# Kernel optimization log

Hardware: AMD Instinct MI355X
Metric: run time of the kernel (lower is better)

## Reference

```python
import jax, jax.numpy as jnp
import numpy as np

N = 65536      # total nodes (cells) in batch
E = 262144     # edges per edge type
T = 3          # edge types: row, col, diag
D = 128        # hidden_dim
HG = 4         # gat_heads
DHG = D // HG  # 32, GAT head dim
HH = 4         # hgt_heads
DHH = D // HH  # 32, HGT head dim
B = 32         # boards per batch
SLOPE = 0.2
EPS = 1e-6


def setup_inputs():
    ks = jax.random.split(jax.random.key(0), 32)
    def nrm(i, shape, s=0.05):
        return (jax.random.normal(ks[i], shape) * s).astype(jnp.float32)
    inp = {
        'x_cell': nrm(0, (N, D), 1.0),
        'z_h': nrm(1, (B, D), 1.0),
        'x_cell_embedded': nrm(2, (N, D), 1.0),
        'edge_index': jax.random.randint(ks[3], (T, 2, E), 0, N, dtype=jnp.int32),
        'batch_size': B,
        # GAT conv 1 (one GATConv per edge type, summed)
        'gat1_W': nrm(4, (T, D, D), 0.09),
        'gat1_asrc': nrm(5, (T, HG, DHG), 0.12),
        'gat1_adst': nrm(6, (T, HG, DHG), 0.12),
        'gat1_b': jnp.zeros((T, D), jnp.float32),
        # GAT conv 2
        'gat2_W': nrm(7, (T, D, D), 0.09),
        'gat2_asrc': nrm(8, (T, HG, DHG), 0.12),
        'gat2_adst': nrm(9, (T, HG, DHG), 0.12),
        'gat2_b': jnp.zeros((T, D), jnp.float32),
        # RMSNorms
        'norm1_s': jnp.ones((D,), jnp.float32),
        'norm2_s': jnp.ones((D,), jnp.float32),
        'norm3_s': jnp.ones((D,), jnp.float32),
        # HGT (single node type 'cell', T edge types)
        'hgt_Wk': nrm(10, (D, D), 0.09), 'hgt_bk': jnp.zeros((D,), jnp.float32),
        'hgt_Wq': nrm(11, (D, D), 0.09), 'hgt_bq': jnp.zeros((D,), jnp.float32),
        'hgt_Wv': nrm(12, (D, D), 0.09), 'hgt_bv': jnp.zeros((D,), jnp.float32),
        'hgt_arel': nrm(13, (T, HH, DHH, DHH), 0.15),
        'hgt_mrel': nrm(14, (T, HH, DHH, DHH), 0.15),
        'hgt_prel': jnp.ones((T, HH), jnp.float32),
        'hgt_Wo': nrm(15, (D, D), 0.09), 'hgt_bo': jnp.zeros((D,), jnp.float32),
        'hgt_skip': jnp.ones((), jnp.float32),
        # input injection
        'inj_W': nrm(16, (D, D), 0.09), 'inj_b': jnp.zeros((D,), jnp.float32),
        # FiLM
        'film_W1': nrm(17, (D, 2 * D), 0.09), 'film_b1': jnp.zeros((2 * D,), jnp.float32),
        'film_W2': nrm(18, (2 * D, 2 * D), 0.001), 'film_b2': jnp.zeros((2 * D,), jnp.float32),
    }
    return inp


def _rmsnorm(x, scale):
    return scale * x * jax.lax.rsqrt(jnp.mean(x * x, axis=-1, keepdims=True) + EPS)


def _res(x_old, x_new, scale):
    return jax.nn.leaky_relu(x_old + _rmsnorm(x_new, scale), SLOPE)


def _gat_sum(x, W, asrc, adst, b, src, dst):
    """HeteroConv(sum) over T GATConvs (concat heads, add_self_loops)."""
    loop = jnp.arange(N, dtype=src.dtype)
    def one(Wt, a_s, a_d, bt, s, t):
        s = jnp.concatenate([s, loop])   # self loops
        t = jnp.concatenate([t, loop])
        h = (x @ Wt).reshape(N, HG, DHG)             # [N,H,Dh]
        alpha_src = (h * a_s).sum(-1)                # [N,H]
        alpha_dst = (h * a_d).sum(-1)
        e = jax.nn.leaky_relu(alpha_src[s] + alpha_dst[t], SLOPE)  # [E+N,H]
        m = jax.ops.segment_max(e, t, num_segments=N)
        ex = jnp.exp(e - m[t])
        denom = jax.ops.segment_sum(ex, t, num_segments=N)
        alpha = ex / (denom[t] + 1e-16)
        out = jax.ops.segment_sum(alpha[:, :, None] * h[s], t, num_segments=N)
        return out.reshape(N, D) + bt
    return jax.vmap(one)(W, asrc, adst, b, src, dst).sum(0)


def _hgt(x, Wk, bk, Wq, bq, Wv, bv, a_rel, m_rel, p_rel, Wo, bo, skip, src, dst):
    k = (x @ Wk + bk).reshape(N, HH, DHH)
    q = (x @ Wq + bq).reshape(N, HH, DHH)
    v = (x @ Wv + bv).reshape(N, HH, DHH)
    # per-edge-type relation transforms at node level, then gather per edge
    k_t = jnp.einsum('nhd,thdf->tnhf', k, a_rel)    # [T,N,H,Dk]
    v_t = jnp.einsum('nhd,thdf->tnhf', v, m_rel)
    k_e = jax.vmap(lambda a, i: a[i])(k_t, src)     # [T,E,H,Dk]
    v_e = jax.vmap(lambda a, i: a[i])(v_t, src)
    score = (q[dst] * k_e).sum(-1) * p_rel[:, None, :] / np.sqrt(DHH)  # [T,E,H]
    score = score.reshape(T * E, HH)
    dst_f = dst.reshape(-1)
    m = jax.ops.segment_max(score, dst_f, num_segments=N)
    ex = jnp.exp(score - m[dst_f])
    denom = jax.ops.segment_sum(ex, dst_f, num_segments=N)
    alpha = ex / (denom[dst_f] + 1e-16)
    agg = jax.ops.segment_sum(alpha[:, :, None] * v_e.reshape(T * E, HH, DHH),
                              dst_f, num_segments=N)          # [N,H,Dk]
    out = jax.nn.gelu(agg.reshape(N, D), approximate=False) @ Wo + bo
    sig = jax.nn.sigmoid(skip)
    return sig * out + (1.0 - sig) * x


def _film(nodes, z_h, W1, b1, W2, b2, bsz):
    gb = jax.nn.gelu(z_h @ W1 + b1, approximate=False) @ W2 + b2  # [B,2D]
    gamma, beta = jnp.split(gb, 2, axis=-1)
    gamma = 0.1 * jnp.tanh(gamma)
    beta = 0.1 * jnp.tanh(beta)
    c = N // bsz
    out = (1.0 + gamma)[:, None, :] * nodes.reshape(bsz, c, D) + beta[:, None, :]
    return out.reshape(N, D)


def reference(x_cell, z_h, x_cell_embedded,
              gat1_W, gat1_asrc, gat1_adst, gat1_b,
              gat2_W, gat2_asrc, gat2_adst, gat2_b,
              norm1_s, norm2_s, norm3_s,
              hgt_Wk, hgt_bk, hgt_Wq, hgt_bq, hgt_Wv, hgt_bv,
              hgt_arel, hgt_mrel, hgt_prel, hgt_Wo, hgt_bo, hgt_skip,
              inj_W, inj_b, film_W1, film_b1, film_W2, film_b2,
              edge_index, batch_size):
    src = edge_index[:, 0]
    dst = edge_index[:, 1]
    x1 = _res(x_cell, _gat_sum(x_cell, gat1_W, gat1_asrc, gat1_adst, gat1_b, src, dst), norm1_s)
    x2 = _res(x1, _gat_sum(x1, gat2_W, gat2_asrc, gat2_adst, gat2_b, src, dst), norm2_s)
    x3 = _res(x2, _hgt(x2, hgt_Wk, hgt_bk, hgt_Wq, hgt_bq, hgt_Wv, hgt_bv,
                       hgt_arel, hgt_mrel, hgt_prel, hgt_Wo, hgt_bo, hgt_skip,
                       src, dst), norm3_s)
    x3 = x3 + x_cell_embedded @ inj_W + inj_b
    return _film(x3, z_h, film_W1, film_b1, film_W2, film_b2, batch_size)
```

## Files before the change

### kernel.cpp

```cpp
#include <hip/hip_runtime.h>

#define NN 65536
#define EE 262144
#define ND ((size_t)NN * 128)
#define TBW 132

typedef unsigned short u16;
typedef short bf8_t __attribute__((ext_vector_type(8)));
typedef float f32x4 __attribute__((ext_vector_type(4)));

__device__ __forceinline__ float lrelu(float x){ return x > 0.f ? x : 0.2f*x; }
__device__ __forceinline__ float gelu_exact(float x){ return 0.5f*x*(1.f+erff(x*0.70710678118654752f)); }
__device__ __forceinline__ u16 f2bf(float f){
    union { float f; unsigned u; } v; v.f = f;
    unsigned u = v.u;
    return (u16)((u + 0x7FFFu + ((u >> 16) & 1u)) >> 16);
}
__device__ __forceinline__ float bf2f(u16 b){
    union { unsigned u; float f; } v; v.u = ((unsigned)b) << 16; return v.f;
}
__device__ __forceinline__ float2 bf2x(unsigned p){
    union { unsigned u; float f; } a, b;
    a.u = (p & 0xFFFFu) << 16; b.u = p & 0xFFFF0000u;
    return make_float2(a.f, b.f);
}
__device__ __forceinline__ unsigned cvt2(float a, float b){
    unsigned r; asm("v_cvt_pk_bf16_f32 %0, %1, %2" : "=v"(r) : "v"(a), "v"(b)); return r;
}

__device__ __forceinline__ void load_af32(const float* __restrict__ X, int row, int lk, bf8_t* af){
    #pragma unroll
    for (int kk = 0; kk < 4; ++kk){
        const float* p = X + (size_t)row*128 + kk*32 + lk*8;
        float4 a = *(const float4*)p;
        float4 b = *(const float4*)(p+4);
        union { bf8_t v; unsigned u[4]; } r;
        r.u[0] = cvt2(a.x, a.y); r.u[1] = cvt2(a.z, a.w);
        r.u[2] = cvt2(b.x, b.y); r.u[3] = cvt2(b.z, b.w);
        af[kk] = r.v;
    }
}
__device__ __forceinline__ void load_af16(const u16* __restrict__ X, int row, int lk, bf8_t* af){
    #pragma unroll
    for (int kk = 0; kk < 4; ++kk)
        af[kk] = *(const bf8_t*)(X + (size_t)row*128 + kk*32 + lk*8);
}
__device__ __forceinline__ void mfma_w1_acc(const bf8_t* af, const u16* __restrict__ Wp,
                                            int lr, int lk, f32x4* acc){
    #pragma unroll
    for (int kk = 0; kk < 4; ++kk){
        bf8_t B[8];
        #pragma unroll
        for (int nt = 0; nt < 8; ++nt)
            B[nt] = *(const bf8_t*)&Wp[(nt*16+lr)*128 + kk*32 + lk*8];
        #pragma unroll
        for (int nt = 0; nt < 8; ++nt)
            acc[nt] = __builtin_amdgcn_mfma_f32_16x16x32_bf16(af[kk], B[nt], acc[nt], 0, 0, 0);
    }
}
__device__ __forceinline__ void mfma_w1(const bf8_t* af, const u16* __restrict__ Wp,
                                        int lr, int lk, f32x4* acc){
    #pragma unroll
    for (int i = 0; i < 8; ++i) acc[i] = (f32x4){0.f,0.f,0.f,0.f};
    mfma_w1_acc(af, Wp, lr, lk, acc);
}
__device__ __forceinline__ void mfma_w2_acc(const bf8_t* af0, const bf8_t* af1,
                                            const u16* __restrict__ Wp,
                                            int lr, int lk, f32x4* acc0, f32x4* acc1){
    #pragma unroll
    for (int kk = 0; kk < 4; ++kk){
        bf8_t B[8];
        #pragma unroll
        for (int nt = 0; nt < 8; ++nt)
            B[nt] = *(const bf8_t*)&Wp[(nt*16+lr)*128 + kk*32 + lk*8];
        #pragma unroll
        for (int nt = 0; nt < 8; ++nt){
            acc0[nt] = __builtin_amdgcn_mfma_f32_16x16x32_bf16(af0[kk], B[nt], acc0[nt], 0, 0, 0);
            acc1[nt] = __builtin_amdgcn_mfma_f32_16x16x32_bf16(af1[kk], B[nt], acc1[nt], 0, 0, 0);
        }
    }
}
__device__ __forceinline__ void mfma_w2(const bf8_t* af0, const bf8_t* af1,
                                        const u16* __restrict__ Wp,
                                        int lr, int lk, f32x4* acc0, f32x4* acc1){
    #pragma unroll
    for (int i = 0; i < 8; ++i){ acc0[i] = (f32x4){0.f,0.f,0.f,0.f}; acc1[i] = (f32x4){0.f,0.f,0.f,0.f}; }
    mfma_w2_acc(af0, af1, Wp, lr, lk, acc0, acc1);
}
__device__ __forceinline__ void acc_to_tb(u16 (*tbw)[TBW], const f32x4* acc, int lr, int lk, const float* bias){
    asm volatile("s_waitcnt lgkmcnt(0)" ::: "memory");
    #pragma unroll
    for (int nt = 0; nt < 8; ++nt){
        int col = nt*16 + lr;
        float badd = bias ? bias[col] : 0.f;
        #pragma unroll
        for (int i = 0; i < 4; ++i) tbw[lk*4+i][col] = f2bf(acc[nt][i] + badd);
    }
    asm volatile("s_waitcnt lgkmcnt(0)" ::: "memory");
}
__device__ __forceinline__ void acc_to_tb_gelu(u16 (*tbw)[TBW], const f32x4* acc, int lr, int lk){
    asm volatile("s_waitcnt lgkmcnt(0)" ::: "memory");
    #pragma unroll
    for (int nt = 0; nt < 8; ++nt){
        int col = nt*16 + lr;
        #pragma unroll
        for (int i = 0; i < 4; ++i) tbw[lk*4+i][col] = f2bf(gelu_exact(acc[nt][i]));
    }
    asm volatile("s_waitcnt lgkmcnt(0)" ::: "memory");
}
__device__ __forceinline__ void tb_store(const u16 (*tbw)[TBW], u16* __restrict__ O, size_t rowstride, int rowbase, int lr, int lk){
    #pragma unroll
    for (int c = 0; c < 4; ++c){
        bf8_t v = *(const bf8_t*)&tbw[c*4+lk][lr*8];
        *(bf8_t*)(O + (size_t)(rowbase + c*4 + lk)*rowstride + lr*8) = v;
    }
}
__device__ __forceinline__ void tb_frags(const u16 (*tbw)[TBW], int lr, int lk, bf8_t* ha){
    #pragma unroll
    for (int kk = 0; kk < 4; ++kk) ha[kk] = *(const bf8_t*)&tbw[lr][kk*32 + lk*8];
}
__device__ __forceinline__ void tb_rows(const u16 (*tbw)[TBW], int lr, int lk, bf8_t* rw){
    #pragma unroll
    for (int c = 0; c < 4; ++c) rw[c] = *(const bf8_t*)&tbw[c*4+lk][lr*8];
}

__global__ __launch_bounds__(256) void wpack_k(
    const float* __restrict__ g1W, const float* __restrict__ g2W,
    const float* __restrict__ Wk, const float* __restrict__ Wq, const float* __restrict__ Wv,
    const float* __restrict__ Wo, const float* __restrict__ injW,
    const float* __restrict__ arel, const float* __restrict__ mrel,
    const float* __restrict__ g1as, const float* __restrict__ g1ad,
    const float* __restrict__ g2as, const float* __restrict__ g2ad,
    u16* __restrict__ wp, u16* __restrict__ wpa)
{
    int b = blockIdx.x, tid = threadIdx.x;
    if (b < 17) {
        const float* src; int rel = 0;
        if (b < 3) src = g1W + b*16384;
        else if (b < 6) src = g2W + (b-3)*16384;
        else if (b == 6) src = Wk;
        else if (b == 7) src = Wq;
        else if (b == 8) src = Wv;
        else if (b == 9) src = Wo;
        else if (b == 10) src = injW;
        else if (b < 14) { src = arel + (b-11)*4096; rel = 2; }
        else { src = mrel + (b-14)*4096; rel = 1; }
        u16* dst = wp + (size_t)b*16384;
        for (int idx = tid; idx < 16384; idx += 256) {
            int n = idx >> 7, k = idx & 127;
            float v;
            if (rel == 1)      v = ((n>>5)==(k>>5)) ? src[(n>>5)*1024 + (k&31)*32 + (n&31)] : 0.f;
            else if (rel == 2) v = ((n>>5)==(k>>5)) ? src[(n>>5)*1024 + (n&31)*32 + (k&31)] : 0.f;
            else               v = src[k*128 + n];
            dst[idx] = f2bf(v);
        }
    } else {
        for (int idx = tid; idx < 6*2048; idx += 256) {
            int m = idx >> 11;
            int j = idx & 2047;
            int cg = j >> 7, k = j & 127;
            const float* as = (m < 3) ? g1as : g2as;
            const float* ad = (m < 3) ? g1ad : g2ad;
            int t = (m < 3) ? m : m - 3;
            float v = 0.f;
            if (cg < 4)      { if ((k>>5)==cg)   v = as[t*128 + cg*32 + (k&31)]; }
            else if (cg < 8) { int g = cg-4; if ((k>>5)==g) v = ad[t*128 + g*32 + (k&31)]; }
            wpa[idx] = f2bf(v);
        }
    }
}

template<int AF32>
__global__ __launch_bounds__(256, 2) void gat_gemm3_k(const float* __restrict__ Xf, const u16* __restrict__ Xb,
    const u16* __restrict__ wpg, const u16* __restrict__ wpa,
    u16* __restrict__ hb, float* __restrict__ alsb, float* __restrict__ aldb)
{
    __shared__ u16 tb[4][16][TBW];
    const int tid = threadIdx.x, wave = tid>>6, lane = tid&63, lr = lane&15, lk = lane>>4;
    const int rw0 = blockIdx.x*128 + wave*32;
    bf8_t af0[4], af1[4];
    if (AF32){ load_af32(Xf, rw0 + lr, lk, af0); load_af32(Xf, rw0 + 16 + lr, lk, af1); }
    else     { load_af16(Xb, rw0 + lr, lk, af0); load_af16(Xb, rw0 + 16 + lr, lk, af1); }
    f32x4 acc0[8], acc1[8];
    for (int t = 0; t < 3; ++t) {
        mfma_w2(af0, af1, wpg + t*16384, lr, lk, acc0, acc1);
        bf8_t Ba[4];
        #pragma unroll
        for (int kk = 0; kk < 4; ++kk)
            Ba[kk] = *(const bf8_t*)&wpa[t*2048 + lr*128 + kk*32 + lk*8];
        u16* h = hb + (size_t)t*ND;
        float* alst = alsb + (size_t)t*NN*4;
        float* aldt = aldb + (size_t)t*NN*4;
        {
            acc_to_tb(tb[wave], acc0, lr, lk, nullptr);
            tb_store(tb[wave], h, 128, rw0, lr, lk);
            bf8_t ha[4]; tb_frags(tb[wave], lr, lk, ha);
            f32x4 a2 = (f32x4){0.f,0.f,0.f,0.f};
            #pragma unroll
            for (int kk = 0; kk < 4; ++kk)
                a2 = __builtin_amdgcn_mfma_f32_16x16x32_bf16(ha[kk], Ba[kk], a2, 0, 0, 0);
            if (lr < 8){
                float* dp = (lr < 4) ? alst : aldt;
                int g = lr & 3;
                #pragma unroll
                for (int i = 0; i < 4; ++i) dp[(size_t)(rw0 + lk*4 + i)*4 + g] = a2[i];
            }
        }
        {
            acc_to_tb(tb[wave], acc1, lr, lk, nullptr);
            tb_store(tb[wave], h, 128, rw0 + 16, lr, lk);
            bf8_t ha[4]; tb_frags(tb[wave], lr, lk, ha);
            f32x4 a2 = (f32x4){0.f,0.f,0.f,0.f};
            #pragma unroll
            for (int kk = 0; kk < 4; ++kk)
                a2 = __builtin_amdgcn_mfma_f32_16x16x32_bf16(ha[kk], Ba[kk], a2, 0, 0, 0);
            if (lr < 8){
                float* dp = (lr < 4) ? alst : aldt;
                int g = lr & 3;
                #pragma unroll
                for (int i = 0; i < 4; ++i) dp[(size_t)(rw0 + 16 + lk*4 + i)*4 + g] = a2[i];
            }
        }
    }
}

__global__ __launch_bounds__(256, 2) void hgt_proj_k(const u16* __restrict__ X,
    const u16* __restrict__ wpk, const u16* __restrict__ wpq, const u16* __restrict__ wpv,
    const u16* __restrict__ wparel,
    const float* __restrict__ bk, const float* __restrict__ bq, const float* __restrict__ bv,
    u16* __restrict__ kvb, u16* __restrict__ qtb)
{
    __shared__ u16 tb[4][16][TBW];
    const int tid = threadIdx.x, wave = tid>>6, lane = tid&63, lr = lane&15, lk = lane>>4;
    const int rw0 = blockIdx.x*128 + wave*32;
    bf8_t af0[4], af1[4];
    load_af16(X, rw0 + lr, lk, af0);
    load_af16(X, rw0 + 16 + lr, lk, af1);
    f32x4 acc0[8], acc1[8];
    mfma_w2(af0, af1, wpk, lr, lk, acc0, acc1);
    acc_to_tb(tb[wave], acc0, lr, lk, bk); tb_store(tb[wave], kvb, 256, rw0, lr, lk);
    acc_to_tb(tb[wave], acc1, lr, lk, bk); tb_store(tb[wave], kvb, 256, rw0 + 16, lr, lk);
    mfma_w2(af0, af1, wpv, lr, lk, acc0, acc1);
    acc_to_tb(tb[wave], acc0, lr, lk, bv); tb_store(tb[wave], kvb + 128, 256, rw0, lr, lk);
    acc_to_tb(tb[wave], acc1, lr, lk, bv); tb_store(tb[wave], kvb + 128, 256, rw0 + 16, lr, lk);
    bf8_t ha0[4], ha1[4];
    mfma_w2(af0, af1, wpq, lr, lk, acc0, acc1);
    acc_to_tb(tb[wave], acc0, lr, lk, bq); tb_frags(tb[wave], lr, lk, ha0);
    acc_to_tb(tb[wave], acc1, lr, lk, bq); tb_frags(tb[wave], lr, lk, ha1);
    for (int t = 0; t < 3; ++t){
        mfma_w2(ha0, ha1, wparel + t*16384, lr, lk, acc0, acc1);
        u16* o = qtb + (size_t)t*ND;
        acc_to_tb(tb[wave], acc0, lr, lk, nullptr); tb_store(tb[wave], o, 128, rw0, lr, lk);
        acc_to_tb(tb[wave], acc1, lr, lk, nullptr); tb_store(tb[wave], o, 128, rw0 + 16, lr, lk);
    }
}

__global__ __launch_bounds__(256) void hgt_agg_k(const u16* __restrict__ kvb,
    const u16* __restrict__ qtb, const float* __restrict__ prel,
    const int* __restrict__ coff, const int* __restrict__ csrc,
    u16* __restrict__ pb)
{
    int gid = blockIdx.x*256 + threadIdx.x;
    int node = gid >> 6, lane = gid & 63;
    int hh = lane >> 4;
    float a0[3], a1[3];
    float dsum = 0.f;
    #pragma unroll
    for (int t = 0; t < 3; ++t) {
        a0[t] = 0.f; a1[t] = 0.f;
        float ph = prel[t*4 + hh] * 0.17677669529663689f;
        float2 qv = bf2x(*(const unsigned*)&qtb[(size_t)t*ND + (size_t)node*128 + lane*2]);
        const int* cs = csrc + (size_t)t*EE;
        int beg = coff[t*(NN+1) + node], end = coff[t*(NN+1) + node + 1];
        int e = beg;
        for (; e + 4 <= end; e += 4) {
            int sA = cs[e], sB = cs[e+1], sC = cs[e+2], sD = cs[e+3];
            size_t rA = (size_t)sA*256 + lane*2, rB = (size_t)sB*256 + lane*2;
            size_t rC = (size_t)sC*256 + lane*2, rD = (size_t)sD*256 + lane*2;
            unsigned kA = *(const unsigned*)&kvb[rA], kB = *(const unsigned*)&kvb[rB];
            unsigned kC = *(const unsigned*)&kvb[rC], kD = *(const unsigned*)&kvb[rD];
            unsigned vA = *(const unsigned*)&kvb[rA+128], vB = *(const unsigned*)&kvb[rB+128];
            unsigned vC = *(const unsigned*)&kvb[rC+128], vD = *(const unsigned*)&kvb[rD+128];
            float2 k2A = bf2x(kA), k2B = bf2x(kB), k2C = bf2x(kC), k2D = bf2x(kD);
            float scA = qv.x*k2A.x + qv.y*k2A.y;
            float scB = qv.x*k2B.x + qv.y*k2B.y;
            float scC = qv.x*k2C.x + qv.y*k2C.y;
            float scD = qv.x*k2D.x + qv.y*k2D.y;
            #pragma unroll
            for (int o = 1; o < 16; o <<= 1){
                scA += __shfl_xor(scA, o); scB += __shfl_xor(scB, o);
                scC += __shfl_xor(scC, o); scD += __shfl_xor(scD, o);
            }
            float eA = expf(scA*ph), eB = expf(scB*ph), eC = expf(scC*ph), eD = expf(scD*ph);
            float2 v2A = bf2x(vA), v2B = bf2x(vB), v2C = bf2x(vC), v2D = bf2x(vD);
            dsum += eA + eB + eC + eD;
            a0[t] += eA*v2A.x + eB*v2B.x + eC*v2C.x + eD*v2D.x;
            a1[t] += eA*v2A.y + eB*v2B.y + eC*v2C.y + eD*v2D.y;
        }
        for (; e < end; ++e) {
            int s = cs[e];
            size_t ro = (size_t)s*256 + lane*2;
            float2 kv = bf2x(*(const unsigned*)&kvb[ro]);
            float sc = qv.x*kv.x + qv.y*kv.y;
            #pragma unroll
            for (int o = 1; o < 16; o <<= 1) sc += __shfl_xor(sc, o);
            float ex = expf(sc * ph);
            float2 vx = bf2x(*(const unsigned*)&kvb[ro + 128]);
            dsum += ex; a0[t] += ex*vx.x; a1[t] += ex*vx.y;
        }
    }
    float inv = 1.f/(dsum + 1e-16f);
    size_t o = (size_t)node*128 + lane*2;
    #pragma unroll
    for (int t = 0; t < 3; ++t)
        *(unsigned*)&pb[(size_t)t*ND + o] = cvt2(a0[t]*inv, a1[t]*inv);
}

__global__ __launch_bounds__(256, 2) void final_k(const u16* __restrict__ pb,
    const u16* __restrict__ wpmrel, const u16* __restrict__ wpo, const float* __restrict__ bo,
    const u16* __restrict__ x2b, const float* __restrict__ skipp, const float* __restrict__ scale,
    const float* __restrict__ xemb, const u16* __restrict__ wpinj, const float* __restrict__ injb,
    const float* __restrict__ gbuf, const int* __restrict__ bszp,
    float* __restrict__ out)
{
    __shared__ u16 tb[4][2][16][TBW];
    const int tid = threadIdx.x, wave = tid>>6, lane = tid&63, lr = lane&15, lk = lane>>4;
    const int rw0 = blockIdx.x*128 + wave*32;
    const int rw1 = rw0 + 16;
    f32x4 acc0[8], acc1[8];
    #pragma unroll
    for (int i = 0; i < 8; ++i){ acc0[i] = (f32x4){0.f,0.f,0.f,0.f}; acc1[i] = (f32x4){0.f,0.f,0.f,0.f}; }
    for (int t = 0; t < 3; ++t){
        bf8_t a0[4], a1[4];
        load_af16(pb + (size_t)t*ND, rw0 + lr, lk, a0);
        load_af16(pb + (size_t)t*ND, rw1 + lr, lk, a1);
        mfma_w2_acc(a0, a1, wpmrel + t*16384, lr, lk, acc0, acc1);
    }
    acc_to_tb_gelu(tb[wave][0], acc0, lr, lk);
    acc_to_tb_gelu(tb[wave][1], acc1, lr, lk);
    bf8_t ga0[4], ga1[4];
    tb_frags(tb[wave][0], lr, lk, ga0);
    tb_frags(tb[wave][1], lr, lk, ga1);
    mfma_w2(ga0, ga1, wpo, lr, lk, acc0, acc1);
    acc_to_tb(tb[wave][0], acc0, lr, lk, bo);
    acc_to_tb(tb[wave][1], acc1, lr, lk, bo);
    bf8_t hw0[4], hw1[4];
    tb_rows(tb[wave][0], lr, lk, hw0);
    tb_rows(tb[wave][1], lr, lk, hw1);
    bf8_t e0[4], e1[4];
    load_af32(xemb, rw0 + lr, lk, e0);
    load_af32(xemb, rw1 + lr, lk, e1);
    mfma_w2(e0, e1, wpinj, lr, lk, acc0, acc1);
    acc_to_tb(tb[wave][0], acc0, lr, lk, injb);
    acc_to_tb(tb[wave][1], acc1, lr, lk, injb);
    bf8_t in0[4], in1[4];
    tb_rows(tb[wave][0], lr, lk, in0);
    tb_rows(tb[wave][1], lr, lk, in1);
    const float sig = 1.f/(1.f + expf(-skipp[0]));
    const int cpb = NN / *bszp;
    float4 sca = *(const float4*)&scale[lr*8];
    float4 scb = *(const float4*)&scale[lr*8 + 4];
    #pragma unroll
    for (int tile = 0; tile < 2; ++tile){
        const bf8_t* hw = tile ? hw1 : hw0;
        const bf8_t* in = tile ? in1 : in0;
        int rwb = tile ? rw1 : rw0;
        #pragma unroll
        for (int c = 0; c < 4; ++c){
            int row = rwb + c*4 + lk;
            bf8_t x8 = *(const bf8_t*)(x2b + (size_t)row*128 + lr*8);
            float x[8], v[8];
            float ssl = 0.f;
            #pragma unroll
            for (int j = 0; j < 8; ++j){
                x[j] = bf2f((u16)x8[j]);
                float h = bf2f((u16)hw[c][j]);
                v[j] = sig*h + (1.f - sig)*x[j];
                ssl += v[j]*v[j];
            }
            ssl += __shfl_xor(ssl, 1); ssl += __shfl_xor(ssl, 2);
            ssl += __shfl_xor(ssl, 4); ssl += __shfl_xor(ssl, 8);
            float rq = rsqrtf(ssl*(1.f/128.f) + 1e-6f);
            const float* gr = gbuf + (row / cpb)*256;
            float4 g0 = *(const float4*)&gr[lr*8];
            float4 g1 = *(const float4*)&gr[lr*8 + 4];
            float4 b0 = *(const float4*)&gr[128 + lr*8];
            float4 b1 = *(const float4*)&gr[128 + lr*8 + 4];
            float4 oA, oB;
            #pragma unroll
            for (int j = 0; j < 8; ++j){
                float scj = (j < 4) ? ((const float*)&sca)[j] : ((const float*)&scb)[j-4];
                float y = lrelu(x[j] + scj*v[j]*rq);
                float hf = y + bf2f((u16)in[c][j]);
                float gj = (j < 4) ? ((const float*)&g0)[j] : ((const float*)&g1)[j-4];
                float bj = (j < 4) ? ((const float*)&b0)[j] : ((const float*)&b1)[j-4];
                float ov = (1.f + gj)*hf + bj;
                if (j < 4) ((float*)&oA)[j] = ov; else ((float*)&oB)[j-4] = ov;
            }
            *(float4*)(out + (size_t)row*128 + lr*8)     = oA;
            *(float4*)(out + (size_t)row*128 + lr*8 + 4) = oB;
        }
    }
}

__global__ __launch_bounds__(256) void hist_k(const int* __restrict__ ei, int* __restrict__ cnt){
    int gid = blockIdx.x*256 + threadIdx.x;
    int t = gid / EE, e = gid - t*EE;
    int d = ei[t*2*EE + EE + e];
    atomicAdd(&cnt[t*NN + d], 1);
}
__global__ __launch_bounds__(256) void scan1_k(const int* __restrict__ cnt, int* __restrict__ off, int* __restrict__ parts){
    __shared__ int sums[256];
    int b = blockIdx.x; int t = b >> 6; int base = (b & 63) * 1024;
    int tid = threadIdx.x;
    int v[4]; int tsum = 0;
    int gbase = t*NN + base + tid*4;
    #pragma unroll
    for (int i = 0; i < 4; ++i){ v[i] = cnt[gbase+i]; tsum += v[i]; }
    sums[tid] = tsum; __syncthreads();
    for (int ofs = 1; ofs < 256; ofs <<= 1) {
        int a = (tid >= ofs) ? sums[tid-ofs] : 0;
        __syncthreads();
        sums[tid] += a;
        __syncthreads();
    }
    int run = sums[tid] - tsum;
    int obase = t*(NN+1) + base + tid*4;
    #pragma unroll
    for (int i = 0; i < 4; ++i){ off[obase+i] = run; run += v[i]; }
    if (tid == 255) parts[b] = sums[255];
}
__global__ void scan2_k(int* parts){
    if (threadIdx.x == 0 && blockIdx.x == 0) {
        for (int t = 0; t < 3; ++t) {
            int run = 0;
            for (int i = 0; i < 64; ++i) { int b = t*64+i; int v = parts[b]; parts[b] = run; run += v; }
        }
    }
}
__global__ __launch_bounds__(256) void scan3_k(int* __restrict__ off, const int* __restrict__ parts){
    int b = blockIdx.x; int t = b >> 6; int base = (b & 63) * 1024;
    int add = parts[b];
    int idx = t*(NN+1) + base + threadIdx.x*4;
    #pragma unroll
    for (int i = 0; i < 4; ++i) off[idx+i] += add;
    if (threadIdx.x == 0 && (b & 63) == 0) off[t*(NN+1) + NN] = EE;
}
__global__ __launch_bounds__(256) void scatter_k(const int* __restrict__ ei, const int* __restrict__ off,
                                                 int* __restrict__ cur, int* __restrict__ out){
    int gid = blockIdx.x*256 + threadIdx.x;
    int t = gid / EE, e = gid - t*EE;
    int s = ei[t*2*EE + e];
    int d = ei[t*2*EE + EE + e];
    int p = atomicAdd(&cur[t*NN + d], 1);
    out[t*EE + off[t*(NN+1)+d] + p] = s;
}

template<int XF32>
__global__ __launch_bounds__(256) void gat_aggres_k(const u16* __restrict__ hb,
    const float* __restrict__ alsb, const float* __restrict__ aldb,
    const int* __restrict__ coff, const int* __restrict__ csrc,
    const float* __restrict__ bias3, const float* __restrict__ xoldf, const u16* __restrict__ xoldb,
    const float* __restrict__ scale, u16* __restrict__ outb)
{
    int gid = blockIdx.x*256 + threadIdx.x;
    int node = gid >> 6, lane = gid & 63;
    int g = lane >> 4;
    float a0 = 0.f, a1 = 0.f;
    for (int t = 0; t < 3; ++t) {
        const u16* h = hb + (size_t)t*ND;
        const float* als = alsb + (size_t)t*NN*4;
        float ad = aldb[(size_t)t*NN*4 + node*4 + g];
        float aself = als[node*4 + g];
        const int* cs = csrc + (size_t)t*EE;
        int beg = coff[t*(NN+1) + node], end = coff[t*(NN+1) + node + 1];
        float ex = expf(lrelu(aself + ad));
        float dsum = ex;
        float2 hv = bf2x(*(const unsigned*)&h[(size_t)node*128 + lane*2]);
        float s0 = ex*hv.x, s1 = ex*hv.y;
        int e = beg;
        for (; e + 4 <= end; e += 4) {
            int sA = cs[e], sB = cs[e+1], sC = cs[e+2], sD = cs[e+3];
            unsigned hA = *(const unsigned*)&h[(size_t)sA*128 + lane*2];
            unsigned hB = *(const unsigned*)&h[(size_t)sB*128 + lane*2];
            unsigned hC = *(const unsigned*)&h[(size_t)sC*128 + lane*2];
            unsigned hD = *(const unsigned*)&h[(size_t)sD*128 + lane*2];
            float aA = als[sA*4+g], aB = als[sB*4+g], aC = als[sC*4+g], aD = als[sD*4+g];
            float eA = expf(lrelu(aA + ad)), eB = expf(lrelu(aB + ad));
            float eC = expf(lrelu(aC + ad)), eD = expf(lrelu(aD + ad));
            float2 wA = bf2x(hA), wB = bf2x(hB), wC = bf2x(hC), wD = bf2x(hD);
            dsum += eA + eB + eC + eD;
            s0 += eA*wA.x + eB*wB.x + eC*wC.x + eD*wD.x;
            s1 += eA*wA.y + eB*wB.y + eC*wC.y + eD*wD.y;
        }
        for (; e < end; ++e) {
            int s = cs[e];
            unsigned hp = *(const unsigned*)&h[(size_t)s*128 + lane*2];
            float av = als[s*4 + g];
            float exx = expf(lrelu(av + ad));
            float2 hw = bf2x(hp);
            dsum += exx; s0 += exx*hw.x; s1 += exx*hw.y;
        }
        float inv = 1.f/(dsum + 1e-16f);
        a0 += s0*inv; a1 += s1*inv;
    }
    int c0 = lane*2;
    a0 += bias3[c0]   + bias3[128+c0]   + bias3[256+c0];
    a1 += bias3[c0+1] + bias3[128+c0+1] + bias3[256+c0+1];
    float ssum = a0*a0 + a1*a1;
    #pragma unroll
    for (int o = 1; o < 64; o <<= 1) ssum += __shfl_xor(ssum, o);
    float r = rsqrtf(ssum*(1.f/128.f) + 1e-6f);
    size_t off = (size_t)node*128 + c0;
    float2 xo;
    if (XF32) xo = *(const float2*)&xoldf[off];
    else      xo = bf2x(*(const unsigned*)&xoldb[off]);
    float y0 = lrelu(xo.x + scale[c0]*a0*r);
    float y1 = lrelu(xo.y + scale[c0+1]*a1*r);
    *(unsigned*)&outb[off] = cvt2(y0, y1);
}

__global__ __launch_bounds__(256) void film_k(const float* __restrict__ z,
    const float* __restrict__ W1, const float* __restrict__ b1,
    const float* __restrict__ W2, const float* __restrict__ b2,
    float* __restrict__ gb)
{
    __shared__ float zr[128];
    __shared__ float g1[256];
    int r = blockIdx.x, tid = threadIdx.x;
    if (tid < 128) zr[tid] = z[r*128 + tid];
    __syncthreads();
    float s = b1[tid];
    for (int k = 0; k < 128; ++k) s += zr[k]*W1[k*256 + tid];
    g1[tid] = gelu_exact(s);
    __syncthreads();
    float s2 = b2[tid];
    for (int k = 0; k < 256; ++k) s2 += g1[k]*W2[k*256 + tid];
    gb[r*256 + tid] = 0.1f*tanhf(s2);
}

extern "C" void kernel_launch(void* const* d_in, const int* in_sizes, int n_in,
                              void* d_out, int out_size, void* d_ws, size_t ws_size,
                              hipStream_t stream)
{
    const float* x_cell = (const float*)d_in[0];
    const float* z_h    = (const float*)d_in[1];
    const float* x_emb  = (const float*)d_in[2];
    const int*   eidx   = (const int*)d_in[3];
    const int*   bszp   = (const int*)d_in[4];
    const float* g1W  = (const float*)d_in[5];
    const float* g1as = (const float*)d_in[6];
    const float* g1ad = (const float*)d_in[7];
    const float* g1b  = (const float*)d_in[8];
    const float* g2W  = (const float*)d_in[9];
    const float* g2as = (const float*)d_in[10];
    const float* g2ad = (const float*)d_in[11];
    const float* g2b  = (const float*)d_in[12];
    const float* n1s  = (const float*)d_in[13];
    const float* n2s  = (const float*)d_in[14];
    const float* n3s  = (const float*)d_in[15];
    const float* Wk   = (const float*)d_in[16];
    const float* bk   = (const float*)d_in[17];
    const float* Wq   = (const float*)d_in[18];
    const float* bq   = (const float*)d_in[19];
    const float* Wv   = (const float*)d_in[20];
    const float* bv   = (const float*)d_in[21];
    const float* arel = (const float*)d_in[22];
    const float* mrel = (const float*)d_in[23];
    const float* prel = (const float*)d_in[24];
    const float* Wo   = (const float*)d_in[25];
    const float* bo   = (const float*)d_in[26];
    const float* skipp= (const float*)d_in[27];
    const float* injW = (const float*)d_in[28];
    const float* injb = (const float*)d_in[29];
    const float* fW1  = (const float*)d_in[30];
    const float* fb1  = (const float*)d_in[31];
    const float* fW2  = (const float*)d_in[32];
    const float* fb2  = (const float*)d_in[33];

    u16* wp   = (u16*)d_ws;
    u16* wpa  = wp + (size_t)17*16384;
    u16* x1b  = wpa + 6*2048;
    u16* x2b  = x1b + ND;
    u16* kvb  = x2b + ND;
    u16* pb   = kvb + 2*ND;
    u16* hb   = pb + 3*ND;
    float* alsb = (float*)(hb + 3*ND);
    float* aldb = alsb + (size_t)3*NN*4;
    float* gbuf = aldb + (size_t)3*NN*4;
    int* coff   = (int*)(gbuf + 32*256);
    int* csrc   = coff + 3*(NN+1);
    int* tmpc   = csrc + 3*EE;
    int* parts  = tmpc + 3*NN;

    u16* qtb = hb;
    float* outp = (float*)d_out;

    const u16* wpg1 = wp;
    const u16* wpg2 = wp + (size_t)3*16384;
    const u16* wpk  = wp + (size_t)6*16384;
    const u16* wpq  = wp + (size_t)7*16384;
    const u16* wpv  = wp + (size_t)8*16384;
    const u16* wpo  = wp + (size_t)9*16384;
    const u16* wpinj= wp + (size_t)10*16384;
    const u16* wparel = wp + (size_t)11*16384;
    const u16* wpmrel = wp + (size_t)14*16384;

    wpack_k<<<18, 256, 0, stream>>>(g1W, g2W, Wk, Wq, Wv, Wo, injW, arel, mrel,
                                    g1as, g1ad, g2as, g2ad, wp, wpa);

    hipMemsetAsync(tmpc, 0, 3*NN*sizeof(int), stream);
    hist_k<<<3*EE/256, 256, 0, stream>>>(eidx, tmpc);
    scan1_k<<<192, 256, 0, stream>>>(tmpc, coff, parts);
    scan2_k<<<1, 64, 0, stream>>>(parts);
    scan3_k<<<192, 256, 0, stream>>>(coff, parts);
    hipMemsetAsync(tmpc, 0, 3*NN*sizeof(int), stream);
    scatter_k<<<3*EE/256, 256, 0, stream>>>(eidx, coff, tmpc, csrc);

    int B = in_sizes[1] / 128;
    film_k<<<B, 256, 0, stream>>>(z_h, fW1, fb1, fW2, fb2, gbuf);

    gat_gemm3_k<1><<<512, 256, 0, stream>>>(x_cell, nullptr, wpg1, wpa, hb, alsb, aldb);
    gat_aggres_k<1><<<16384, 256, 0, stream>>>(hb, alsb, aldb, coff, csrc, g1b, x_cell, nullptr, n1s, x1b);

    gat_gemm3_k<0><<<512, 256, 0, stream>>>(nullptr, x1b, wpg2, wpa + 3*2048, hb, alsb, aldb);
    gat_aggres_k<0><<<16384, 256, 0, stream>>>(hb, alsb, aldb, coff, csrc, g2b, nullptr, x1b, n2s, x2b);

    hgt_proj_k<<<512, 256, 0, stream>>>(x2b, wpk, wpq, wpv, wparel,
                                        bk, bq, bv, kvb, qtb);
    hgt_agg_k<<<16384, 256, 0, stream>>>(kvb, qtb, prel, coff, csrc, pb);

    final_k<<<512, 256, 0, stream>>>(pb, wpmrel, wpo, bo, x2b, skipp, n3s,
                                     x_emb, wpinj, injb, gbuf, bszp, outp);
}
```

Baseline: 639.1 us.

## Stage weight matrices in padded shared memory for MFMA GEMM kernels

Before each 128x128 bf16 weight product, the block cooperatively copies the weight matrix into a padded LDS buffer, and the MFMA B fragments are then read from LDS instead of global memory. Previously every wave loaded the same weight fragments from global/L2 on its own. This adds block-wide barriers around each staging step and about 35KB of extra LDS per block, which may limit occupancy under the two-blocks-per-CU launch bound. final_k also shrinks its tile buffer to one per wave by interleaving the conversion and readback of the two tiles.

Result: faster. 572.5 us (-10.4%).

```diff
diff --git a/kernel.cpp b/kernel.cpp
--- a/kernel.cpp
+++ b/kernel.cpp
@@ -4,6 +4,7 @@
 #define EE 262144
 #define ND ((size_t)NN * 128)
 #define TBW 132
+#define WLP 136
 
 typedef unsigned short u16;
 typedef short bf8_t __attribute__((ext_vector_type(8)));
@@ -45,34 +46,38 @@
     for (int kk = 0; kk < 4; ++kk)
         af[kk] = *(const bf8_t*)(X + (size_t)row*128 + kk*32 + lk*8);
 }
-__device__ __forceinline__ void mfma_w1_acc(const bf8_t* af, const u16* __restrict__ Wp,
+
+__device__ __forceinline__ void stage_w(const u16* __restrict__ src, u16* __restrict__ wl, int tid){
+    #pragma unroll
+    for (int j = 0; j < 8; ++j){
+        int o = (j*256 + tid)*8;
+        bf8_t v = *(const bf8_t*)(src + o);
+        *(bf8_t*)(wl + ((o>>7)*WLP + (o&127))) = v;
+    }
+}
+
+__device__ __forceinline__ void mfma_l1_acc(const bf8_t* af, const u16* __restrict__ wl,
                                             int lr, int lk, f32x4* acc){
     #pragma unroll
     for (int kk = 0; kk < 4; ++kk){
         bf8_t B[8];
         #pragma unroll
         for (int nt = 0; nt < 8; ++nt)
-            B[nt] = *(const bf8_t*)&Wp[(nt*16+lr)*128 + kk*32 + lk*8];
+            B[nt] = *(const bf8_t*)&wl[(nt*16+lr)*WLP + kk*32 + lk*8];
         #pragma unroll
         for (int nt = 0; nt < 8; ++nt)
             acc[nt] = __builtin_amdgcn_mfma_f32_16x16x32_bf16(af[kk], B[nt], acc[nt], 0, 0, 0);
     }
 }
-__device__ __forceinline__ void mfma_w1(const bf8_t* af, const u16* __restrict__ Wp,
-                                        int lr, int lk, f32x4* acc){
-    #pragma unroll
-    for (int i = 0; i < 8; ++i) acc[i] = (f32x4){0.f,0.f,0.f,0.f};
-    mfma_w1_acc(af, Wp, lr, lk, acc);
-}
-__device__ __forceinline__ void mfma_w2_acc(const bf8_t* af0, const bf8_t* af1,
-                                            const u16* __restrict__ Wp,
+__device__ __forceinline__ void mfma_l2_acc(const bf8_t* af0, const bf8_t* af1,
+                                            const u16* __restrict__ wl,
                                             int lr, int lk, f32x4* acc0, f32x4* acc1){
     #pragma unroll
     for (int kk = 0; kk < 4; ++kk){
         bf8_t B[8];
         #pragma unroll
         for (int nt = 0; nt < 8; ++nt)
-            B[nt] = *(const bf8_t*)&Wp[(nt*16+lr)*128 + kk*32 + lk*8];
+            B[nt] = *(const bf8_t*)&wl[(nt*16+lr)*WLP + kk*32 + lk*8];
         #pragma unroll
         for (int nt = 0; nt < 8; ++nt){
             acc0[nt] = __builtin_amdgcn_mfma_f32_16x16x32_bf16(af0[kk], B[nt], acc0[nt], 0, 0, 0);
@@ -80,13 +85,14 @@
         }
     }
 }
-__device__ __forceinline__ void mfma_w2(const bf8_t* af0, const bf8_t* af1,
-                                        const u16* __restrict__ Wp,
+__device__ __forceinline__ void mfma_l2(const bf8_t* af0, const bf8_t* af1,
+                                        const u16* __restrict__ wl,
                                         int lr, int lk, f32x4* acc0, f32x4* acc1){
     #pragma unroll
     for (int i = 0; i < 8; ++i){ acc0[i] = (f32x4){0.f,0.f,0.f,0.f}; acc1[i] = (f32x4){0.f,0.f,0.f,0.f}; }
-    mfma_w2_acc(af0, af1, Wp, lr, lk, acc0, acc1);
-}
+    mfma_l2_acc(af0, af1, wl, lr, lk, acc0, acc1);
+}
+
 __device__ __forceinline__ void acc_to_tb(u16 (*tbw)[TBW], const f32x4* acc, int lr, int lk, const float* bias){
     asm volatile("s_waitcnt lgkmcnt(0)" ::: "memory");
     #pragma unroll
@@ -175,7 +181,8 @@
     const u16* __restrict__ wpg, const u16* __restrict__ wpa,
     u16* __restrict__ hb, float* __restrict__ alsb, float* __restrict__ aldb)
 {
-    __shared__ u16 tb[4][16][TBW];
+    __shared__ __align__(16) u16 wl[128*WLP];
+    __shared__ __align__(16) u16 tb[4][16][TBW];
     const int tid = threadIdx.x, wave = tid>>6, lane = tid&63, lr = lane&15, lk = lane>>4;
     const int rw0 = blockIdx.x*128 + wave*32;
     bf8_t af0[4], af1[4];
@@ -183,7 +190,10 @@
     else     { load_af16(Xb, rw0 + lr, lk, af0); load_af16(Xb, rw0 + 16 + lr, lk, af1); }
     f32x4 acc0[8], acc1[8];
     for (int t = 0; t < 3; ++t) {
-        mfma_w2(af0, af1, wpg + t*16384, lr, lk, acc0, acc1);
+        __syncthreads();
+        stage_w(wpg + t*16384, wl, tid);
+        __syncthreads();
+        mfma_l2(af0, af1, wl, lr, lk, acc0, acc1);
         bf8_t Ba[4];
         #pragma unroll
         for (int kk = 0; kk < 4; ++kk)
@@ -230,25 +240,37 @@
     const float* __restrict__ bk, const float* __restrict__ bq, const float* __restrict__ bv,
     u16* __restrict__ kvb, u16* __restrict__ qtb)
 {
-    __shared__ u16 tb[4][16][TBW];
+    __shared__ __align__(16) u16 wl[128*WLP];
+    __shared__ __align__(16) u16 tb[4][16][TBW];
     const int tid = threadIdx.x, wave = tid>>6, lane = tid&63, lr = lane&15, lk = lane>>4;
     const int rw0 = blockIdx.x*128 + wave*32;
     bf8_t af0[4], af1[4];
     load_af16(X, rw0 + lr, lk, af0);
     load_af16(X, rw0 + 16 + lr, lk, af1);
     f32x4 acc0[8], acc1[8];
-    mfma_w2(af0, af1, wpk, lr, lk, acc0, acc1);
+    stage_w(wpk, wl, tid);
+    __syncthreads();
+    mfma_l2(af0, af1, wl, lr, lk, acc0, acc1);
     acc_to_tb(tb[wave], acc0, lr, lk, bk); tb_store(tb[wave], kvb, 256, rw0, lr, lk);
     acc_to_tb(tb[wave], acc1, lr, lk, bk); tb_store(tb[wave], kvb, 256, rw0 + 16, lr, lk);
-    mfma_w2(af0, af1, wpv, lr, lk, acc0, acc1);
+    __syncthreads();
+    stage_w(wpv, wl, tid);
+    __syncthreads();
+    mfma_l2(af0, af1, wl, lr, lk, acc0, acc1);
     acc_to_tb(tb[wave], acc0, lr, lk, bv); tb_store(tb[wave], kvb + 128, 256, rw0, lr, lk);
     acc_to_tb(tb[wave], acc1, lr, lk, bv); tb_store(tb[wave], kvb + 128, 256, rw0 + 16, lr, lk);
+    __syncthreads();
+    stage_w(wpq, wl, tid);
+    __syncthreads();
     bf8_t ha0[4], ha1[4];
-    mfma_w2(af0, af1, wpq, lr, lk, acc0, acc1);
+    mfma_l2(af0, af1, wl, lr, lk, acc0, acc1);
     acc_to_tb(tb[wave], acc0, lr, lk, bq); tb_frags(tb[wave], lr, lk, ha0);
     acc_to_tb(tb[wave], acc1, lr, lk, bq); tb_frags(tb[wave], lr, lk, ha1);
     for (int t = 0; t < 3; ++t){
-        mfma_w2(ha0, ha1, wparel + t*16384, lr, lk, acc0, acc1);
+        __syncthreads();
+        stage_w(wparel + t*16384, wl, tid);
+        __syncthreads();
+        mfma_l2(ha0, ha1, wl, lr, lk, acc0, acc1);
         u16* o = qtb + (size_t)t*ND;
         acc_to_tb(tb[wave], acc0, lr, lk, nullptr); tb_store(tb[wave], o, 128, rw0, lr, lk);
         acc_to_tb(tb[wave], acc1, lr, lk, nullptr); tb_store(tb[wave], o, 128, rw0 + 16, lr, lk);
@@ -323,7 +345,8 @@
     const float* __restrict__ gbuf, const int* __restrict__ bszp,
     float* __restrict__ out)
 {
-    __shared__ u16 tb[4][2][16][TBW];
+    __shared__ __align__(16) u16 wl[128*WLP];
+    __shared__ __align__(16) u16 tb[4][16][TBW];
     const int tid = threadIdx.x, wave = tid>>6, lane = tid&63, lr = lane&15, lk = lane>>4;
     const int rw0 = blockIdx.x*128 + wave*32;
     const int rw1 = rw0 + 16;
@@ -331,31 +354,40 @@
     #pragma unroll
     for (int i = 0; i < 8; ++i){ acc0[i] = (f32x4){0.f,0.f,0.f,0.f}; acc1[i] = (f32x4){0.f,0.f,0.f,0.f}; }
     for (int t = 0; t < 3; ++t){
+        if (t) __syncthreads();
+        stage_w(wpmrel + t*16384, wl, tid);
+        __syncthreads();
         bf8_t a0[4], a1[4];
         load_af16(pb + (size_t)t*ND, rw0 + lr, lk, a0);
         load_af16(pb + (size_t)t*ND, rw1 + lr, lk, a1);
-        mfma_w2_acc(a0, a1, wpmrel + t*16384, lr, lk, acc0, acc1);
-    }
-    acc_to_tb_gelu(tb[wave][0], acc0, lr, lk);
-    acc_to_tb_gelu(tb[wave][1], acc1, lr, lk);
+        mfma_l2_acc(a0, a1, wl, lr, lk, acc0, acc1);
+    }
     bf8_t ga0[4], ga1[4];
-    tb_frags(tb[wave][0], lr, lk, ga0);
-    tb_frags(tb[wave][1], lr, lk, ga1);
-    mfma_w2(ga0, ga1, wpo, lr, lk, acc0, acc1);
-    acc_to_tb(tb[wave][0], acc0, lr, lk, bo);
-    acc_to_tb(tb[wave][1], acc1, lr, lk, bo);
+    acc_to_tb_gelu(tb[wave], acc0, lr, lk);
+    tb_frags(tb[wave], lr, lk, ga0);
+    acc_to_tb_gelu(tb[wave], acc1, lr, lk);
+    tb_frags(tb[wave], lr, lk, ga1);
+    __syncthreads();
+    stage_w(wpo, wl, tid);
+    __syncthreads();
+    mfma_l2(ga0, ga1, wl, lr, lk, acc0, acc1);
     bf8_t hw0[4], hw1[4];
-    tb_rows(tb[wave][0], lr, lk, hw0);
-    tb_rows(tb[wave][1], lr, lk, hw1);
+    acc_to_tb(tb[wave], acc0, lr, lk, bo);
+    tb_rows(tb[wave], lr, lk, hw0);
+    acc_to_tb(tb[wave], acc1, lr, lk, bo);
+    tb_rows(tb[wave], lr, lk, hw1);
     bf8_t e0[4], e1[4];
     load_af32(xemb, rw0 + lr, lk, e0);
     load_af32(xemb, rw1 + lr, lk, e1);
-    mfma_w2(e0, e1, wpinj, lr, lk, acc0, acc1);
-    acc_to_tb(tb[wave][0], acc0, lr, lk, injb);
-    acc_to_tb(tb[wave][1], acc1, lr, lk, injb);
+    __syncthreads();
+    stage_w(wpinj, wl, tid);
+    __syncthreads();
+    mfma_l2(e0, e1, wl, lr, lk, acc0, acc1);
     bf8_t in0[4], in1[4];
-    tb_rows(tb[wave][0], lr, lk, in0);
-    tb_rows(tb[wave][1], lr, lk, in1);
+    acc_to_tb(tb[wave], acc0, lr, lk, injb);
+    tb_rows(tb[wave], lr, lk, in0);
+    acc_to_tb(tb[wave], acc1, lr, lk, injb);
+    tb_rows(tb[wave], lr, lk, in1);
     const float sig = 1.f/(1.f + expf(-skipp[0]));
     const int cpb = NN / *bszp;
     float4 sca = *(const float4*)&scale[lr*8];
```
